# Performance work log

Measured on AMD Instinct MI355X. Metric: run time of the kernel, lower is better.

Reference implementation:

```python
import jax, jax.numpy as jnp
import numpy as np

NUM_ROUTING = 3

def _squash(s):
    # squared_norm * s / ((1 + squared_norm) * sqrt(squared_norm)), norm over last dim
    sn = jnp.sum(s * s, axis=-1, keepdims=True)
    return sn * s / ((1.0 + sn) * jnp.sqrt(sn))

def setup_inputs() -> dict:
    key = jax.random.key(0)
    kx, kw = jax.random.split(key)
    B, IN_CAPS, IN_DIM, OUT_CAPS, OUT_DIM = 64, 8192, 8, 8, 16
    x = jax.random.normal(kx, (B, IN_CAPS, IN_DIM), dtype=jnp.float32)
    W = 0.01 * jax.random.normal(kw, (IN_CAPS, OUT_CAPS, IN_DIM, OUT_DIM), dtype=jnp.float32)
    return {"x": x, "W": W}

def reference(x, W):
    # x: [B, in_caps, in_dim]; W: [in_caps, out_caps, in_dim, out_dim]
    u_hat = jnp.einsum('ijnm,bin->bijm', W, x)          # [B, i, j, m]
    temp_u_hat = jax.lax.stop_gradient(u_hat)           # detach, routing uses no grads
    B, I, J = x.shape[0], W.shape[0], W.shape[1]
    b = jnp.zeros((B, I, J), dtype=x.dtype)
    for _ in range(NUM_ROUTING - 1):
        c = jax.nn.softmax(b, axis=2)                   # over out_caps j
        s = jnp.einsum('bij,bijm->bjm', c, temp_u_hat)  # [B, j, m]
        v = _squash(s)
        b = b + jnp.einsum('bjm,bijm->bij', v, temp_u_hat)  # agreement
    c = jax.nn.softmax(b, axis=2)
    s = jnp.einsum('bij,bijm->bjm', c, u_hat)
    return _squash(s)                                   # [B, out_caps, out_dim]
```

## Files before the change

### kernel.cpp

```cpp
#include <hip/hip_runtime.h>


#define BB      64
#define ICAPS   8192
#define NDIM    8
#define JCAPS   8
#define MDIM    16
#define NBLK    256
#define ICHUNK  (ICAPS / NBLK)
#define IG      8
#define NSTAGE  (ICHUNK / IG)
#define WJ_STRIDE 136
#define WI_STRIDE (JCAPS * WJ_STRIDE)
#define S_ELEMS  (BB * JCAPS * MDIM)

template <int CTRL>
__device__ __forceinline__ float dpp_xadd(float v) {
    const int p = __builtin_amdgcn_mov_dpp(__float_as_int(v), CTRL, 0xF, 0xF, true);
    return v + __int_as_float(p);
}
#define DPP_XOR1 0xB1
#define DPP_XOR2 0x4E
#define DPP_ROR4 0x124
#define DPP_ROR8 0x128

template <int MODE>
__global__ __launch_bounds__(512, 1)
void caps_pass_kernel(
    const float* __restrict__ x, const float* __restrict__ W,
    const float* __restrict__ vsum, float* __restrict__ partial)
{
    __shared__ float Wlds[IG * WI_STRIDE];

    const int tid = threadIdx.x;
    const int mq  = tid & 3;
    const int j   = (tid >> 2) & 7;
    const int bq  = tid >> 5;
    const int blk = blockIdx.x;
    const int i0  = blk * ICHUNK;

    float s[4][4];
    #pragma unroll
    for (int k = 0; k < 4; ++k)
        #pragma unroll
        for (int m = 0; m < 4; ++m) s[k][m] = 0.f;

    float v[4][4];
    if (MODE == 1) {
        #pragma unroll
        for (int k = 0; k < 4; ++k) {
            const float4 a = *(const float4*)
                &vsum[((bq + 16 * k) * JCAPS + j) * MDIM + mq * 4];
            v[k][0] = a.x; v[k][1] = a.y; v[k][2] = a.z; v[k][3] = a.w;
        }
    }

    for (int st = 0; st < NSTAGE; ++st) {
        {
            const int iL  = tid >> 6;
            const int rem = tid & 63;
            const float4* src = (const float4*)(W + (size_t)(i0 + st * IG + iL) * 1024
                                                  + rem * 16);
            float4* dst = (float4*)&Wlds[iL * WI_STRIDE + (rem >> 3) * WJ_STRIDE
                                         + (rem & 7) * 16];
            dst[0] = src[0]; dst[1] = src[1]; dst[2] = src[2]; dst[3] = src[3];
        }
        __syncthreads();

        #pragma unroll
        for (int ii = 0; ii < IG; ++ii) {
            const int i = i0 + st * IG + ii;

            float u[4][4];
            #pragma unroll
            for (int k = 0; k < 4; ++k)
                #pragma unroll
                for (int m = 0; m < 4; ++m) u[k][m] = 0.f;
            const float* wb = &Wlds[ii * WI_STRIDE + j * WJ_STRIDE + mq * 4];

            {
                float4 xa[4];
                #pragma unroll
                for (int k = 0; k < 4; ++k)
                    xa[k] = *(const float4*)&x[((size_t)(bq + 16 * k) * ICAPS + i) * NDIM];
                #pragma unroll
                for (int n = 0; n < 4; ++n) {
                    const float4 wq = *(const float4*)&wb[n * MDIM];
                    #pragma unroll
                    for (int k = 0; k < 4; ++k) {
                        const float xn = (n == 0) ? xa[k].x : (n == 1) ? xa[k].y
                                       : (n == 2) ? xa[k].z : xa[k].w;
                        u[k][0] += xn * wq.x; u[k][1] += xn * wq.y;
                        u[k][2] += xn * wq.z; u[k][3] += xn * wq.w;
                    }
                }
            }
            {
                float4 xb[4];
                #pragma unroll
                for (int k = 0; k < 4; ++k)
                    xb[k] = *(const float4*)&x[((size_t)(bq + 16 * k) * ICAPS + i) * NDIM + 4];
                #pragma unroll
                for (int n = 0; n < 4; ++n) {
                    const float4 wq = *(const float4*)&wb[(n + 4) * MDIM];
                    #pragma unroll
                    for (int k = 0; k < 4; ++k) {
                        const float xn = (n == 0) ? xb[k].x : (n == 1) ? xb[k].y
                                       : (n == 2) ? xb[k].z : xb[k].w;
                        u[k][0] += xn * wq.x; u[k][1] += xn * wq.y;
                        u[k][2] += xn * wq.z; u[k][3] += xn * wq.w;
                    }
                }
            }

            if (MODE == 0) {
                #pragma unroll
                for (int k = 0; k < 4; ++k)
                    #pragma unroll
                    for (int m = 0; m < 4; ++m) s[k][m] += u[k][m];
            } else {
                float lp[4];
                #pragma unroll
                for (int k = 0; k < 4; ++k)
                    lp[k] = u[k][0] * v[k][0] + u[k][1] * v[k][1]
                          + u[k][2] * v[k][2] + u[k][3] * v[k][3];
                #pragma unroll
                for (int k = 0; k < 4; ++k) lp[k] = dpp_xadd<DPP_XOR1>(lp[k]);
                #pragma unroll
                for (int k = 0; k < 4; ++k) lp[k] = dpp_xadd<DPP_XOR2>(lp[k]);
                float e[4], d[4];
                #pragma unroll
                for (int k = 0; k < 4; ++k) { e[k] = __expf(lp[k]); }
                #pragma unroll
                for (int k = 0; k < 4; ++k) d[k] = dpp_xadd<DPP_ROR4>(e[k]);
                #pragma unroll
                for (int k = 0; k < 4; ++k) d[k] = dpp_xadd<DPP_ROR8>(d[k]);
                #pragma unroll
                for (int k = 0; k < 4; ++k) d[k] += __shfl_xor(d[k], 16);
                #pragma unroll
                for (int k = 0; k < 4; ++k) {
                    const float c = e[k] * __builtin_amdgcn_rcpf(d[k]);
                    #pragma unroll
                    for (int m = 0; m < 4; ++m) s[k][m] += c * u[k][m];
                }
            }
        }
        __syncthreads();
    }

    const float sc = (MODE == 0) ? 0.125f : 1.0f;
    float* pp = partial + (size_t)blk * S_ELEMS;
    #pragma unroll
    for (int k = 0; k < 4; ++k) {
        float4 o;
        o.x = s[k][0] * sc; o.y = s[k][1] * sc;
        o.z = s[k][2] * sc; o.w = s[k][3] * sc;
        *(float4*)&pp[((bq + 16 * k) * JCAPS + j) * MDIM + mq * 4] = o;
    }
}

template <int OP>
__global__ __launch_bounds__(256) void caps_reduce_kernel(
    const float* __restrict__ partial, float* __restrict__ vsum, float* __restrict__ out)
{
    __shared__ float sd[256];
    const int bo  = blockIdx.x;
    const int tid = threadIdx.x;
    const int kg  = tid >> 6;
    const int tl  = tid & 63;
    const int t   = bo * 64 + tl;

    float a0 = 0.f, a1 = 0.f, a2 = 0.f, a3 = 0.f;
    const float* p = partial + (size_t)kg * 64 * S_ELEMS + t;
    #pragma unroll
    for (int k = 0; k < 64; k += 4) {
        a0 += p[(size_t)(k + 0) * S_ELEMS];
        a1 += p[(size_t)(k + 1) * S_ELEMS];
        a2 += p[(size_t)(k + 2) * S_ELEMS];
        a3 += p[(size_t)(k + 3) * S_ELEMS];
    }
    sd[tid] = (a0 + a1) + (a2 + a3);
    __syncthreads();

    if (tid < 64) {
        const float s = (sd[tid] + sd[64 + tid]) + (sd[128 + tid] + sd[192 + tid]);
        float sn = s * s;
        sn += __shfl_xor(sn, 1);
        sn += __shfl_xor(sn, 2);
        sn += __shfl_xor(sn, 4);
        sn += __shfl_xor(sn, 8);
        const float v = s * sqrtf(sn) / (1.f + sn);
        const int tt = bo * 64 + tid;
        if (OP == 2)      out[tt]   = v;
        else if (OP == 1) vsum[tt] += v;
        else              vsum[tt]  = v;
    }
}

extern "C" void kernel_launch(void* const* d_in, const int* in_sizes, int n_in,
                              void* d_out, int out_size, void* d_ws, size_t ws_size,
                              hipStream_t stream)
{
    const float* x = (const float*)d_in[0];
    const float* W = (const float*)d_in[1];
    float* out = (float*)d_out;

    float* partial = (float*)d_ws;
    float* vsum    = partial + (size_t)NBLK * S_ELEMS;

    caps_pass_kernel<0><<<NBLK, 512, 0, stream>>>(x, W, vsum, partial);
    caps_reduce_kernel<0><<<128, 256, 0, stream>>>(partial, vsum, nullptr);
    caps_pass_kernel<1><<<NBLK, 512, 0, stream>>>(x, W, vsum, partial);
    caps_reduce_kernel<1><<<128, 256, 0, stream>>>(partial, vsum, nullptr);
    caps_pass_kernel<1><<<NBLK, 512, 0, stream>>>(x, W, vsum, partial);
    caps_reduce_kernel<2><<<128, 256, 0, stream>>>(partial, vsum, out);
}
```

Baseline: 184.9 us.

## Stage x tiles in LDS and split input capsules across more blocks

```diff
diff --git a/kernel.cpp b/kernel.cpp
--- a/kernel.cpp
+++ b/kernel.cpp
@@ -6,12 +6,10 @@
 #define NDIM    8
 #define JCAPS   8
 #define MDIM    16
-#define NBLK    256
-#define ICHUNK  (ICAPS / NBLK)
 #define IG      8
-#define NSTAGE  (ICHUNK / IG)
 #define WJ_STRIDE 136
 #define WI_STRIDE (JCAPS * WJ_STRIDE)
+#define XB_STRIDE 68
 #define S_ELEMS  (BB * JCAPS * MDIM)
 
 template <int CTRL>
@@ -24,20 +22,21 @@
 #define DPP_ROR4 0x124
 #define DPP_ROR8 0x128
 
-template <int MODE>
+template <int MODE, int NCH>
 __global__ __launch_bounds__(512, 1)
 void caps_pass_kernel(
     const float* __restrict__ x, const float* __restrict__ W,
     const float* __restrict__ vsum, float* __restrict__ partial)
 {
     __shared__ float Wlds[IG * WI_STRIDE];
+    __shared__ float Xlds[BB * XB_STRIDE];
 
     const int tid = threadIdx.x;
     const int mq  = tid & 3;
     const int j   = (tid >> 2) & 7;
     const int bq  = tid >> 5;
     const int blk = blockIdx.x;
-    const int i0  = blk * ICHUNK;
+    const int i0  = blk * NCH;
 
     float s[4][4];
     #pragma unroll
@@ -55,7 +54,7 @@
         }
     }
 
-    for (int st = 0; st < NSTAGE; ++st) {
+    for (int st = 0; st < NCH / IG; ++st) {
         {
             const int iL  = tid >> 6;
             const int rem = tid & 63;
@@ -65,52 +64,50 @@
                                          + (rem & 7) * 16];
             dst[0] = src[0]; dst[1] = src[1]; dst[2] = src[2]; dst[3] = src[3];
         }
+        {
+            const int tb = tid >> 3;
+            const int tn = tid & 7;
+            const float4* src = (const float4*)(x + ((size_t)tb * ICAPS + i0 + st * IG)
+                                                      * NDIM + tn * 8);
+            float4* dst = (float4*)&Xlds[tb * XB_STRIDE + tn * 8];
+            dst[0] = src[0]; dst[1] = src[1];
+        }
         __syncthreads();
 
         #pragma unroll
         for (int ii = 0; ii < IG; ++ii) {
-            const int i = i0 + st * IG + ii;
+            const float* wb = &Wlds[ii * WI_STRIDE + j * WJ_STRIDE + mq * 4];
+            float4 w0 = *(const float4*)&wb[0 * MDIM];
+            float4 w1 = *(const float4*)&wb[1 * MDIM];
+            float4 w2 = *(const float4*)&wb[2 * MDIM];
+            float4 w3 = *(const float4*)&wb[3 * MDIM];
+            float4 w4 = *(const float4*)&wb[4 * MDIM];
+            float4 w5 = *(const float4*)&wb[5 * MDIM];
+            float4 w6 = *(const float4*)&wb[6 * MDIM];
+            float4 w7 = *(const float4*)&wb[7 * MDIM];
 
             float u[4][4];
             #pragma unroll
-            for (int k = 0; k < 4; ++k)
-                #pragma unroll
-                for (int m = 0; m < 4; ++m) u[k][m] = 0.f;
-            const float* wb = &Wlds[ii * WI_STRIDE + j * WJ_STRIDE + mq * 4];
-
-            {
-                float4 xa[4];
-                #pragma unroll
-                for (int k = 0; k < 4; ++k)
-                    xa[k] = *(const float4*)&x[((size_t)(bq + 16 * k) * ICAPS + i) * NDIM];
-                #pragma unroll
-                for (int n = 0; n < 4; ++n) {
-                    const float4 wq = *(const float4*)&wb[n * MDIM];
-                    #pragma unroll
-                    for (int k = 0; k < 4; ++k) {
-                        const float xn = (n == 0) ? xa[k].x : (n == 1) ? xa[k].y
-                                       : (n == 2) ? xa[k].z : xa[k].w;
-                        u[k][0] += xn * wq.x; u[k][1] += xn * wq.y;
-                        u[k][2] += xn * wq.z; u[k][3] += xn * wq.w;
-                    }
-                }
-            }
-            {
-                float4 xb[4];
-                #pragma unroll
-                for (int k = 0; k < 4; ++k)
-                    xb[k] = *(const float4*)&x[((size_t)(bq + 16 * k) * ICAPS + i) * NDIM + 4];
-                #pragma unroll
-                for (int n = 0; n < 4; ++n) {
-                    const float4 wq = *(const float4*)&wb[(n + 4) * MDIM];
-                    #pragma unroll
-                    for (int k = 0; k < 4; ++k) {
-                        const float xn = (n == 0) ? xb[k].x : (n == 1) ? xb[k].y
-                                       : (n == 2) ? xb[k].z : xb[k].w;
-                        u[k][0] += xn * wq.x; u[k][1] += xn * wq.y;
-                        u[k][2] += xn * wq.z; u[k][3] += xn * wq.w;
-                    }
-                }
+            for (int k = 0; k < 4; ++k) {
+                const float* xp = &Xlds[(bq + 16 * k) * XB_STRIDE + ii * 8];
+                const float4 xA = *(const float4*)xp;
+                const float4 xB = *(const float4*)(xp + 4);
+                u[k][0]  = xA.x * w0.x; u[k][1]  = xA.x * w0.y;
+                u[k][2]  = xA.x * w0.z; u[k][3]  = xA.x * w0.w;
+                u[k][0] += xA.y * w1.x; u[k][1] += xA.y * w1.y;
+                u[k][2] += xA.y * w1.z; u[k][3] += xA.y * w1.w;
+                u[k][0] += xA.z * w2.x; u[k][1] += xA.z * w2.y;
+                u[k][2] += xA.z * w2.z; u[k][3] += xA.z * w2.w;
+                u[k][0] += xA.w * w3.x; u[k][1] += xA.w * w3.y;
+                u[k][2] += xA.w * w3.z; u[k][3] += xA.w * w3.w;
+                u[k][0] += xB.x * w4.x; u[k][1] += xB.x * w4.y;
+                u[k][2] += xB.x * w4.z; u[k][3] += xB.x * w4.w;
+                u[k][0] += xB.y * w5.x; u[k][1] += xB.y * w5.y;
+                u[k][2] += xB.y * w5.z; u[k][3] += xB.y * w5.w;
+                u[k][0] += xB.z * w6.x; u[k][1] += xB.z * w6.y;
+                u[k][2] += xB.z * w6.z; u[k][3] += xB.z * w6.w;
+                u[k][0] += xB.w * w7.x; u[k][1] += xB.w * w7.y;
+                u[k][2] += xB.w * w7.z; u[k][3] += xB.w * w7.w;
             }
 
             if (MODE == 0) {
@@ -161,7 +158,8 @@
 
 template <int OP>
 __global__ __launch_bounds__(256) void caps_reduce_kernel(
-    const float* __restrict__ partial, float* __restrict__ vsum, float* __restrict__ out)
+    const float* __restrict__ partial, float* __restrict__ vsum,
+    float* __restrict__ out, int npg)
 {
     __shared__ float sd[256];
     const int bo  = blockIdx.x;
@@ -171,9 +169,8 @@
     const int t   = bo * 64 + tl;
 
     float a0 = 0.f, a1 = 0.f, a2 = 0.f, a3 = 0.f;
-    const float* p = partial + (size_t)kg * 64 * S_ELEMS + t;
-    #pragma unroll
-    for (int k = 0; k < 64; k += 4) {
+    const float* p = partial + (size_t)kg * npg * S_ELEMS + t;
+    for (int k = 0; k < npg; k += 4) {
         a0 += p[(size_t)(k + 0) * S_ELEMS];
         a1 += p[(size_t)(k + 1) * S_ELEMS];
         a2 += p[(size_t)(k + 2) * S_ELEMS];
@@ -205,13 +202,26 @@
     const float* W = (const float*)d_in[1];
     float* out = (float*)d_out;
 
+    const bool big = ws_size >= (size_t)(512 + 1) * S_ELEMS * sizeof(float);
+    const int NP   = big ? 512 : 256;
+    const int npg  = NP / 4;
+
     float* partial = (float*)d_ws;
-    float* vsum    = partial + (size_t)NBLK * S_ELEMS;
-
-    caps_pass_kernel<0><<<NBLK, 512, 0, stream>>>(x, W, vsum, partial);
-    caps_reduce_kernel<0><<<128, 256, 0, stream>>>(partial, vsum, nullptr);
-    caps_pass_kernel<1><<<NBLK, 512, 0, stream>>>(x, W, vsum, partial);
-    caps_reduce_kernel<1><<<128, 256, 0, stream>>>(partial, vsum, nullptr);
-    caps_pass_kernel<1><<<NBLK, 512, 0, stream>>>(x, W, vsum, partial);
-    caps_reduce_kernel<2><<<128, 256, 0, stream>>>(partial, vsum, out);
-}
+    float* vsum    = partial + (size_t)NP * S_ELEMS;
+
+    if (big) {
+        caps_pass_kernel<0, 16><<<512, 512, 0, stream>>>(x, W, vsum, partial);
+        caps_reduce_kernel<0><<<128, 256, 0, stream>>>(partial, vsum, nullptr, npg);
+        caps_pass_kernel<1, 16><<<512, 512, 0, stream>>>(x, W, vsum, partial);
+        caps_reduce_kernel<1><<<128, 256, 0, stream>>>(partial, vsum, nullptr, npg);
+        caps_pass_kernel<1, 16><<<512, 512, 0, stream>>>(x, W, vsum, partial);
+        caps_reduce_kernel<2><<<128, 256, 0, stream>>>(partial, vsum, out, npg);
+    } else {
+        caps_pass_kernel<0, 32><<<256, 512, 0, stream>>>(x, W, vsum, partial);
+        caps_reduce_kernel<0><<<128, 256, 0, stream>>>(partial, vsum, nullptr, npg);
+        caps_pass_kernel<1, 32><<<256, 512, 0, stream>>>(x, W, vsum, partial);
+        caps_reduce_kernel<1><<<128, 256, 0, stream>>>(partial, vsum, nullptr, npg);
+        caps_pass_kernel<1, 32><<<256, 512, 0, stream>>>(x, W, vsum, partial);
+        caps_reduce_kernel<2><<<128, 256, 0, stream>>>(partial, vsum, out, npg);
+    }
+}
```

Result: slower. 244.9 us (+32.4%).

## Stage x tiles in LDS and double block count when workspace allows

Applied to the files above, without the earlier changes.

```diff
diff --git a/kernel.cpp b/kernel.cpp
--- a/kernel.cpp
+++ b/kernel.cpp
@@ -6,12 +6,10 @@
 #define NDIM    8
 #define JCAPS   8
 #define MDIM    16
-#define NBLK    256
-#define ICHUNK  (ICAPS / NBLK)
 #define IG      8
-#define NSTAGE  (ICHUNK / IG)
 #define WJ_STRIDE 136
 #define WI_STRIDE (JCAPS * WJ_STRIDE)
+#define XB_STRIDE 68
 #define S_ELEMS  (BB * JCAPS * MDIM)
 
 template <int CTRL>
@@ -24,20 +22,21 @@
 #define DPP_ROR4 0x124
 #define DPP_ROR8 0x128
 
-template <int MODE>
+template <int MODE, int NCH>
 __global__ __launch_bounds__(512, 1)
 void caps_pass_kernel(
     const float* __restrict__ x, const float* __restrict__ W,
     const float* __restrict__ vsum, float* __restrict__ partial)
 {
     __shared__ float Wlds[IG * WI_STRIDE];
+    __shared__ float Xlds[BB * XB_STRIDE];
 
     const int tid = threadIdx.x;
     const int mq  = tid & 3;
     const int j   = (tid >> 2) & 7;
     const int bq  = tid >> 5;
     const int blk = blockIdx.x;
-    const int i0  = blk * ICHUNK;
+    const int i0  = blk * NCH;
 
     float s[4][4];
     #pragma unroll
@@ -55,7 +54,13 @@
         }
     }
 
-    for (int st = 0; st < NSTAGE; ++st) {
+    const float* wjb = &Wlds[j * WJ_STRIDE + mq * 4];
+    const float* xb0 = &Xlds[(bq +  0) * XB_STRIDE];
+    const float* xb1 = &Xlds[(bq + 16) * XB_STRIDE];
+    const float* xb2 = &Xlds[(bq + 32) * XB_STRIDE];
+    const float* xb3 = &Xlds[(bq + 48) * XB_STRIDE];
+
+    for (int st = 0; st < NCH / IG; ++st) {
         {
             const int iL  = tid >> 6;
             const int rem = tid & 63;
@@ -65,24 +70,32 @@
                                          + (rem & 7) * 16];
             dst[0] = src[0]; dst[1] = src[1]; dst[2] = src[2]; dst[3] = src[3];
         }
+        {
+            const int tb = tid >> 3;
+            const int tn = tid & 7;
+            const float4* src = (const float4*)(x + ((size_t)tb * ICAPS + i0 + st * IG)
+                                                      * NDIM + tn * 8);
+            float4* dst = (float4*)&Xlds[tb * XB_STRIDE + tn * 8];
+            dst[0] = src[0]; dst[1] = src[1];
+        }
         __syncthreads();
 
         #pragma unroll
         for (int ii = 0; ii < IG; ++ii) {
-            const int i = i0 + st * IG + ii;
+            const float* wb = wjb + ii * WI_STRIDE;
 
             float u[4][4];
             #pragma unroll
             for (int k = 0; k < 4; ++k)
                 #pragma unroll
                 for (int m = 0; m < 4; ++m) u[k][m] = 0.f;
-            const float* wb = &Wlds[ii * WI_STRIDE + j * WJ_STRIDE + mq * 4];
 
             {
                 float4 xa[4];
-                #pragma unroll
-                for (int k = 0; k < 4; ++k)
-                    xa[k] = *(const float4*)&x[((size_t)(bq + 16 * k) * ICAPS + i) * NDIM];
+                xa[0] = *(const float4*)(xb0 + ii * 8);
+                xa[1] = *(const float4*)(xb1 + ii * 8);
+                xa[2] = *(const float4*)(xb2 + ii * 8);
+                xa[3] = *(const float4*)(xb3 + ii * 8);
                 #pragma unroll
                 for (int n = 0; n < 4; ++n) {
                     const float4 wq = *(const float4*)&wb[n * MDIM];
@@ -97,9 +110,10 @@
             }
             {
                 float4 xb[4];
-                #pragma unroll
-                for (int k = 0; k < 4; ++k)
-                    xb[k] = *(const float4*)&x[((size_t)(bq + 16 * k) * ICAPS + i) * NDIM + 4];
+                xb[0] = *(const float4*)(xb0 + ii * 8 + 4);
+                xb[1] = *(const float4*)(xb1 + ii * 8 + 4);
+                xb[2] = *(const float4*)(xb2 + ii * 8 + 4);
+                xb[3] = *(const float4*)(xb3 + ii * 8 + 4);
                 #pragma unroll
                 for (int n = 0; n < 4; ++n) {
                     const float4 wq = *(const float4*)&wb[(n + 4) * MDIM];
@@ -161,19 +175,19 @@
 
 template <int OP>
 __global__ __launch_bounds__(256) void caps_reduce_kernel(
-    const float* __restrict__ partial, float* __restrict__ vsum, float* __restrict__ out)
+    const float* __restrict__ partial, float* __restrict__ vsum,
+    float* __restrict__ out, int npg)
 {
     __shared__ float sd[256];
     const int bo  = blockIdx.x;
     const int tid = threadIdx.x;
-    const int kg  = tid >> 6;
-    const int tl  = tid & 63;
-    const int t   = bo * 64 + tl;
+    const int kg  = tid >> 5;
+    const int tl  = tid & 31;
+    const int t   = bo * 32 + tl;
 
     float a0 = 0.f, a1 = 0.f, a2 = 0.f, a3 = 0.f;
-    const float* p = partial + (size_t)kg * 64 * S_ELEMS + t;
-    #pragma unroll
-    for (int k = 0; k < 64; k += 4) {
+    const float* p = partial + (size_t)kg * npg * S_ELEMS + t;
+    for (int k = 0; k < npg; k += 4) {
         a0 += p[(size_t)(k + 0) * S_ELEMS];
         a1 += p[(size_t)(k + 1) * S_ELEMS];
         a2 += p[(size_t)(k + 2) * S_ELEMS];
@@ -182,15 +196,17 @@
     sd[tid] = (a0 + a1) + (a2 + a3);
     __syncthreads();
 
-    if (tid < 64) {
-        const float s = (sd[tid] + sd[64 + tid]) + (sd[128 + tid] + sd[192 + tid]);
+    if (tid < 32) {
+        float s = 0.f;
+        #pragma unroll
+        for (int q = 0; q < 8; ++q) s += sd[q * 32 + tid];
         float sn = s * s;
         sn += __shfl_xor(sn, 1);
         sn += __shfl_xor(sn, 2);
         sn += __shfl_xor(sn, 4);
         sn += __shfl_xor(sn, 8);
         const float v = s * sqrtf(sn) / (1.f + sn);
-        const int tt = bo * 64 + tid;
+        const int tt = bo * 32 + tid;
         if (OP == 2)      out[tt]   = v;
         else if (OP == 1) vsum[tt] += v;
         else              vsum[tt]  = v;
@@ -205,13 +221,26 @@
     const float* W = (const float*)d_in[1];
     float* out = (float*)d_out;
 
+    const bool big = ws_size >= (size_t)(512 + 1) * S_ELEMS * sizeof(float);
+    const int NP   = big ? 512 : 256;
+    const int npg  = NP / 8;
+
     float* partial = (float*)d_ws;
-    float* vsum    = partial + (size_t)NBLK * S_ELEMS;
-
-    caps_pass_kernel<0><<<NBLK, 512, 0, stream>>>(x, W, vsum, partial);
-    caps_reduce_kernel<0><<<128, 256, 0, stream>>>(partial, vsum, nullptr);
-    caps_pass_kernel<1><<<NBLK, 512, 0, stream>>>(x, W, vsum, partial);
-    caps_reduce_kernel<1><<<128, 256, 0, stream>>>(partial, vsum, nullptr);
-    caps_pass_kernel<1><<<NBLK, 512, 0, stream>>>(x, W, vsum, partial);
-    caps_reduce_kernel<2><<<128, 256, 0, stream>>>(partial, vsum, out);
-}
+    float* vsum    = partial + (size_t)NP * S_ELEMS;
+
+    if (big) {
+        caps_pass_kernel<0, 16><<<512, 512, 0, stream>>>(x, W, vsum, partial);
+        caps_reduce_kernel<0><<<256, 256, 0, stream>>>(partial, vsum, nullptr, npg);
+        caps_pass_kernel<1, 16><<<512, 512, 0, stream>>>(x, W, vsum, partial);
+        caps_reduce_kernel<1><<<256, 256, 0, stream>>>(partial, vsum, nullptr, npg);
+        caps_pass_kernel<1, 16><<<512, 512, 0, stream>>>(x, W, vsum, partial);
+        caps_reduce_kernel<2><<<256, 256, 0, stream>>>(partial, vsum, out, npg);
+    } else {
+        caps_pass_kernel<0, 32><<<256, 512, 0, stream>>>(x, W, vsum, partial);
+        caps_reduce_kernel<0><<<256, 256, 0, stream>>>(partial, vsum, nullptr, npg);
+        caps_pass_kernel<1, 32><<<256, 512, 0, stream>>>(x, W, vsum, partial);
+        caps_reduce_kernel<1><<<256, 256, 0, stream>>>(partial, vsum, nullptr, npg);
+        caps_pass_kernel<1, 32><<<256, 512, 0, stream>>>(x, W, vsum, partial);
+        caps_reduce_kernel<2><<<256, 256, 0, stream>>>(partial, vsum, out, npg);
+    }
+}
```

Measured after the change: 237.0 us. +28.2%, slower.
